# Optimization experiments

Measured on AMD Instinct MI355X. Metric: run time of the kernel, lower is better.

## Reference

```python
import jax, jax.numpy as jnp
import numpy as np

N = 65536   # nodes
D = 64      # feature dim
K = 32      # top-k kept features per node (k_value)
DEG = 16    # average degree
E = N * DEG # edges


def setup_inputs() -> dict:
    key = jax.random.key(0)
    k1, k2, k3, k4, k5 = jax.random.split(key, 5)
    feat = jax.random.normal(k1, (N, D), dtype=jnp.float32)
    topk_values = jax.random.normal(k2, (N, K), dtype=jnp.float32)
    topk_indices = jax.random.randint(k3, (N, K), 0, D, dtype=jnp.int32)
    edge_src = jax.random.randint(k4, (E,), 0, N, dtype=jnp.int32)
    # sorted dst row ids == CSR row structure (expanded indptr)
    edge_dst = jnp.sort(jax.random.randint(k5, (E,), 0, N, dtype=jnp.int32))
    eps = jnp.zeros((1,), dtype=jnp.float32)  # init_eps=0, learn_eps=False
    return {"feat": feat, "topk_values": topk_values, "eps": eps,
            "topk_indices": topk_indices, "edge_src": edge_src, "edge_dst": edge_dst}


def reference(feat, topk_values, eps, topk_indices, edge_src, edge_dst):
    n, d = feat.shape
    # MaxK SpMM: reconstruct sparse (top-k compressed) dense features, then
    # CSR sum-aggregation with unit edge values (graph_values = ones).
    rows = jnp.arange(n, dtype=topk_indices.dtype)[:, None]        # [N,1]
    dense = jnp.zeros_like(feat).at[rows, topk_indices].add(topk_values)  # [N,D]
    # neigh[i] = sum_{j in N(i)} dense[j]
    neigh = jax.ops.segment_sum(dense[edge_src], edge_dst, num_segments=n)  # [N,D]
    # GIN update: (1 + eps) * feat_dst + neigh  (apply_func=None, activation=None)
    return (1.0 + eps) * feat + neigh
```

## Files before the change

### kernel.cpp

```cpp
#include <hip/hip_runtime.h>


#define DFEAT 64
#define KTOP  32

__device__ __forceinline__ unsigned short f2bf(float x) {
    unsigned u = __float_as_uint(x);
    u += 0x7fffu + ((u >> 16) & 1u);
    return (unsigned short)(u >> 16);
}
__device__ __forceinline__ float bfu(unsigned int u16) {
    return __uint_as_float(u16 << 16);
}

__global__ __launch_bounds__(256) void prep_kernel(
    const float* __restrict__ topk_v,
    const int*   __restrict__ topk_i,
    const int*   __restrict__ edge_dst,
    unsigned int* __restrict__ dense16,
    int*          __restrict__ indptr,
    int n_nodes, int n_edges)
{
    __shared__ float rows[4][2 * DFEAT];
    int tid    = blockIdx.x * blockDim.x + threadIdx.x;
    int stride = gridDim.x * blockDim.x;
    int lane   = threadIdx.x & 63;
    int wid    = threadIdx.x >> 6;
    int wave   = tid >> 6;
    int nwaves = stride >> 6;
    int half   = lane >> 5;

    for (int e = tid; e < n_edges; e += stride) {
        int cur  = edge_dst[e];
        int prev = (e == 0) ? -1 : edge_dst[e - 1];
        for (int node = prev + 1; node <= cur; ++node) indptr[node] = e;
        if (e == n_edges - 1) {
            for (int node = cur + 1; node <= n_nodes; ++node) indptr[node] = n_edges;
        }
    }

    int total_pairs = n_nodes >> 1;
    for (int pair = wave; pair < total_pairs; pair += nwaves) {
        int nodeA = pair * 2;

        rows[wid][lane]      = 0.0f;
        rows[wid][lane + 64] = 0.0f;

        size_t base = (size_t)nodeA * KTOP;
        int   idx = topk_i[base + lane];
        float val = topk_v[base + lane];
        atomicAdd(&rows[wid][half * DFEAT + idx], val);

        float a = rows[wid][2 * lane];
        float b = rows[wid][2 * lane + 1];
        dense16[nodeA * 32 + lane] =
            (unsigned int)f2bf(a) | ((unsigned int)f2bf(b) << 16);
    }
}

__global__ __launch_bounds__(256) void aggregate_bf16_kernel(
    const uint4*  __restrict__ d16q,
    const float4* __restrict__ feat4,
    const float*  __restrict__ eps,
    const int*    __restrict__ edge_src,
    const int*    __restrict__ indptr,
    float4*       __restrict__ out4,
    int n_nodes)
{
    int lane = threadIdx.x & 63;
    int f    = lane & 7;
    int slot = lane >> 3;
    int wave = (blockIdx.x * blockDim.x + threadIdx.x) >> 6;
    int node = wave * 8 + slot;
    if (node >= n_nodes) return;

    float sc = 1.0f + eps[0];
    int s = indptr[node];
    int e = indptr[node + 1];

    float acc[8] = {0, 0, 0, 0, 0, 0, 0, 0};
    for (int base = s; base < e; base += 4) {
#pragma unroll
        for (int u = 0; u < 4; ++u) {
            int ee = base + u;
            if (ee < e) {
                int src = edge_src[ee];
                uint4 r = d16q[(size_t)src * 8 + f];
                acc[0] += bfu(r.x & 0xffffu); acc[1] += bfu(r.x >> 16);
                acc[2] += bfu(r.y & 0xffffu); acc[3] += bfu(r.y >> 16);
                acc[4] += bfu(r.z & 0xffffu); acc[5] += bfu(r.z >> 16);
                acc[6] += bfu(r.w & 0xffffu); acc[7] += bfu(r.w >> 16);
            }
        }
    }

    float4 ft0 = feat4[(size_t)node * 16 + 2 * f];
    float4 ft1 = feat4[(size_t)node * 16 + 2 * f + 1];
    float4 o0, o1;
    o0.x = sc * ft0.x + acc[0];
    o0.y = sc * ft0.y + acc[1];
    o0.z = sc * ft0.z + acc[2];
    o0.w = sc * ft0.w + acc[3];
    o1.x = sc * ft1.x + acc[4];
    o1.y = sc * ft1.y + acc[5];
    o1.z = sc * ft1.z + acc[6];
    o1.w = sc * ft1.w + acc[7];
    out4[(size_t)node * 16 + 2 * f]     = o0;
    out4[(size_t)node * 16 + 2 * f + 1] = o1;
}

extern "C" void kernel_launch(void* const* d_in, const int* in_sizes, int n_in,
                              void* d_out, int out_size, void* d_ws, size_t ws_size,
                              hipStream_t stream)
{
    const float* feat     = (const float*)d_in[0];
    const float* topk_v   = (const float*)d_in[1];
    const float* eps      = (const float*)d_in[2];
    const int*   topk_i   = (const int*)d_in[3];
    const int*   edge_src = (const int*)d_in[4];
    const int*   edge_dst = (const int*)d_in[5];
    float*       out      = (float*)d_out;

    int n_nodes = in_sizes[0] / DFEAT;
    int n_edges = in_sizes[4];

    unsigned int* dense16 = (unsigned int*)d_ws;
    size_t d16_bytes = (size_t)n_nodes * DFEAT * sizeof(unsigned short);
    size_t d16_pad   = (d16_bytes + 255) & ~(size_t)255;
    int*   indptr    = (int*)((char*)d_ws + d16_pad);

    prep_kernel<<<2048, 256, 0, stream>>>(topk_v, topk_i, edge_dst,
                                          dense16, indptr, n_nodes, n_edges);

    int agg_waves  = (n_nodes + 7) / 8;
    int agg_blocks = (agg_waves * 64 + 255) / 256;
    aggregate_bf16_kernel<<<agg_blocks, 256, 0, stream>>>(
        (const uint4*)dense16, (const float4*)feat, eps, edge_src,
        indptr, (float4*)out, n_nodes);
}
```

Before: 124.5 us.

## Fuse prep and aggregation into one cooperative kernel with grid sync

Merges the CSR/dense-building prep kernel and the bf16 aggregation kernel into a single cooperative launch separated by a grid-wide barrier. The aim is to remove the second kernel launch and the inter-kernel gap. The cost is a grid sync. It also requires all 2048 blocks to be co-resident, which constrains registers and could make the launch fail.

Result: slower. 289.5 us (+132.5%).

```diff
diff --git a/kernel.cpp b/kernel.cpp
--- a/kernel.cpp
+++ b/kernel.cpp
@@ -1,4 +1,7 @@
 #include <hip/hip_runtime.h>
+#include <hip/hip_cooperative_groups.h>
+
+namespace cg = cooperative_groups;
 
 
 #define DFEAT 64
@@ -13,12 +16,16 @@
     return __uint_as_float(u16 << 16);
 }
 
-__global__ __launch_bounds__(256) void prep_kernel(
-    const float* __restrict__ topk_v,
-    const int*   __restrict__ topk_i,
-    const int*   __restrict__ edge_dst,
+__global__ __launch_bounds__(256, 8) void fused_kernel(
+    const float*  __restrict__ topk_v,
+    const int*    __restrict__ topk_i,
+    const int*    __restrict__ edge_dst,
+    const int*    __restrict__ edge_src,
+    const float4* __restrict__ feat4,
+    const float*  __restrict__ eps,
     unsigned int* __restrict__ dense16,
     int*          __restrict__ indptr,
+    float4*       __restrict__ out4,
     int n_nodes, int n_edges)
 {
     __shared__ float rows[4][2 * DFEAT];
@@ -28,7 +35,6 @@
     int wid    = threadIdx.x >> 6;
     int wave   = tid >> 6;
     int nwaves = stride >> 6;
-    int half   = lane >> 5;
 
     for (int e = tid; e < n_edges; e += stride) {
         int cur  = edge_dst[e];
@@ -39,87 +45,84 @@
         }
     }
 
-    int total_pairs = n_nodes >> 1;
-    for (int pair = wave; pair < total_pairs; pair += nwaves) {
-        int nodeA = pair * 2;
+    {
+        int half = lane >> 5;
+        int total_pairs = n_nodes >> 1;
+        for (int pair = wave; pair < total_pairs; pair += nwaves) {
+            int nodeA = pair * 2;
 
-        rows[wid][lane]      = 0.0f;
-        rows[wid][lane + 64] = 0.0f;
+            rows[wid][lane]      = 0.0f;
+            rows[wid][lane + 64] = 0.0f;
 
-        size_t base = (size_t)nodeA * KTOP;
-        int   idx = topk_i[base + lane];
-        float val = topk_v[base + lane];
-        atomicAdd(&rows[wid][half * DFEAT + idx], val);
+            size_t base = (size_t)nodeA * KTOP;
+            int   idx = topk_i[base + lane];
+            float val = topk_v[base + lane];
+            atomicAdd(&rows[wid][half * DFEAT + idx], val);
 
-        float a = rows[wid][2 * lane];
-        float b = rows[wid][2 * lane + 1];
-        dense16[nodeA * 32 + lane] =
-            (unsigned int)f2bf(a) | ((unsigned int)f2bf(b) << 16);
-    }
-}
-
-__global__ __launch_bounds__(256) void aggregate_bf16_kernel(
-    const uint4*  __restrict__ d16q,
-    const float4* __restrict__ feat4,
-    const float*  __restrict__ eps,
-    const int*    __restrict__ edge_src,
-    const int*    __restrict__ indptr,
-    float4*       __restrict__ out4,
-    int n_nodes)
-{
-    int lane = threadIdx.x & 63;
-    int f    = lane & 7;
-    int slot = lane >> 3;
-    int wave = (blockIdx.x * blockDim.x + threadIdx.x) >> 6;
-    int node = wave * 8 + slot;
-    if (node >= n_nodes) return;
-
-    float sc = 1.0f + eps[0];
-    int s = indptr[node];
-    int e = indptr[node + 1];
-
-    float acc[8] = {0, 0, 0, 0, 0, 0, 0, 0};
-    for (int base = s; base < e; base += 4) {
-#pragma unroll
-        for (int u = 0; u < 4; ++u) {
-            int ee = base + u;
-            if (ee < e) {
-                int src = edge_src[ee];
-                uint4 r = d16q[(size_t)src * 8 + f];
-                acc[0] += bfu(r.x & 0xffffu); acc[1] += bfu(r.x >> 16);
-                acc[2] += bfu(r.y & 0xffffu); acc[3] += bfu(r.y >> 16);
-                acc[4] += bfu(r.z & 0xffffu); acc[5] += bfu(r.z >> 16);
-                acc[6] += bfu(r.w & 0xffffu); acc[7] += bfu(r.w >> 16);
-            }
+            float a = rows[wid][2 * lane];
+            float b = rows[wid][2 * lane + 1];
+            dense16[nodeA * 32 + lane] =
+                (unsigned int)f2bf(a) | ((unsigned int)f2bf(b) << 16);
         }
     }
 
-    float4 ft0 = feat4[(size_t)node * 16 + 2 * f];
-    float4 ft1 = feat4[(size_t)node * 16 + 2 * f + 1];
-    float4 o0, o1;
-    o0.x = sc * ft0.x + acc[0];
-    o0.y = sc * ft0.y + acc[1];
-    o0.z = sc * ft0.z + acc[2];
-    o0.w = sc * ft0.w + acc[3];
-    o1.x = sc * ft1.x + acc[4];
-    o1.y = sc * ft1.y + acc[5];
-    o1.z = sc * ft1.z + acc[6];
-    o1.w = sc * ft1.w + acc[7];
-    out4[(size_t)node * 16 + 2 * f]     = o0;
-    out4[(size_t)node * 16 + 2 * f + 1] = o1;
+    cg::this_grid().sync();
+
+    const uint4* d16q = (const uint4*)dense16;
+    int f    = lane & 7;
+    int slot = lane >> 3;
+    float sc = 1.0f + eps[0];
+
+    for (int g = wave; g * 8 < n_nodes; g += nwaves) {
+        int node = g * 8 + slot;
+        if (node < n_nodes) {
+            int s = indptr[node];
+            int e = indptr[node + 1];
+
+            float acc[8] = {0, 0, 0, 0, 0, 0, 0, 0};
+            for (int base = s; base < e; base += 4) {
+#pragma unroll
+                for (int u = 0; u < 4; ++u) {
+                    int ee = base + u;
+                    if (ee < e) {
+                        int src = edge_src[ee];
+                        uint4 r = d16q[(size_t)src * 8 + f];
+                        acc[0] += bfu(r.x & 0xffffu); acc[1] += bfu(r.x >> 16);
+                        acc[2] += bfu(r.y & 0xffffu); acc[3] += bfu(r.y >> 16);
+                        acc[4] += bfu(r.z & 0xffffu); acc[5] += bfu(r.z >> 16);
+                        acc[6] += bfu(r.w & 0xffffu); acc[7] += bfu(r.w >> 16);
+                    }
+                }
+            }
+
+            float4 ft0 = feat4[(size_t)node * 16 + 2 * f];
+            float4 ft1 = feat4[(size_t)node * 16 + 2 * f + 1];
+            float4 o0, o1;
+            o0.x = sc * ft0.x + acc[0];
+            o0.y = sc * ft0.y + acc[1];
+            o0.z = sc * ft0.z + acc[2];
+            o0.w = sc * ft0.w + acc[3];
+            o1.x = sc * ft1.x + acc[4];
+            o1.y = sc * ft1.y + acc[5];
+            o1.z = sc * ft1.z + acc[6];
+            o1.w = sc * ft1.w + acc[7];
+            out4[(size_t)node * 16 + 2 * f]     = o0;
+            out4[(size_t)node * 16 + 2 * f + 1] = o1;
+        }
+    }
 }
 
 extern "C" void kernel_launch(void* const* d_in, const int* in_sizes, int n_in,
                               void* d_out, int out_size, void* d_ws, size_t ws_size,
                               hipStream_t stream)
 {
-    const float* feat     = (const float*)d_in[0];
-    const float* topk_v   = (const float*)d_in[1];
-    const float* eps      = (const float*)d_in[2];
-    const int*   topk_i   = (const int*)d_in[3];
-    const int*   edge_src = (const int*)d_in[4];
-    const int*   edge_dst = (const int*)d_in[5];
-    float*       out      = (float*)d_out;
+    const float*  feat     = (const float*)d_in[0];
+    const float*  topk_v   = (const float*)d_in[1];
+    const float*  eps      = (const float*)d_in[2];
+    const int*    topk_i   = (const int*)d_in[3];
+    const int*    edge_src = (const int*)d_in[4];
+    const int*    edge_dst = (const int*)d_in[5];
+    float4*       out      = (float4*)d_out;
 
     int n_nodes = in_sizes[0] / DFEAT;
     int n_edges = in_sizes[4];
@@ -129,12 +132,12 @@
     size_t d16_pad   = (d16_bytes + 255) & ~(size_t)255;
     int*   indptr    = (int*)((char*)d_ws + d16_pad);
 
-    prep_kernel<<<2048, 256, 0, stream>>>(topk_v, topk_i, edge_dst,
-                                          dense16, indptr, n_nodes, n_edges);
-
-    int agg_waves  = (n_nodes + 7) / 8;
-    int agg_blocks = (agg_waves * 64 + 255) / 256;
-    aggregate_bf16_kernel<<<agg_blocks, 256, 0, stream>>>(
-        (const uint4*)dense16, (const float4*)feat, eps, edge_src,
-        indptr, (float4*)out, n_nodes);
+    const float4* feat4 = (const float4*)feat;
+    void* args[] = {
+        (void*)&topk_v, (void*)&topk_i, (void*)&edge_dst, (void*)&edge_src,
+        (void*)&feat4, (void*)&eps, (void*)&dense16, (void*)&indptr,
+        (void*)&out, (void*)&n_nodes, (void*)&n_edges,
+    };
+    hipLaunchCooperativeKernel((const void*)fused_kernel, dim3(2048), dim3(256),
+                               args, 0, stream);
 }
```
